# Kernel optimization log

Hardware: AMD Instinct MI355X
Metric: run time of the kernel (lower is better)

## Reference

```python
import jax, jax.numpy as jnp
import numpy as np

N = 50000          # nodes
E = 800000         # edges (before self loops)
C_IN, HID, C_OUT, L = 128, 64, 64, 3
LSTM_H = (L * HID) // 2   # 96, PyG JK-LSTM hidden size
NEG_SLOPE = 0.2


def gat_conv(x, src, dst, W, a_src, a_dst, b):
    # single-head PyG GATConv
    h = x @ W.T                                  # [N, HID]
    al = h @ a_src                               # [N] src attention logits
    ar = h @ a_dst                               # [N]
    e = jax.nn.leaky_relu(al[src] + ar[dst], NEG_SLOPE)   # [E+N]
    m = jax.ops.segment_max(e, dst, num_segments=N)
    ex = jnp.exp(e - m[dst])
    den = jax.ops.segment_sum(ex, dst, num_segments=N)
    coef = ex / den[dst]                         # segment softmax over dst neighborhoods
    out = jax.ops.segment_sum(coef[:, None] * h[src], dst, num_segments=N)
    return out + b


def lstm_dir(seq, Wih, Whh, bih, bhh, reverse):
    # seq: [L, N, C]; returns hidden states [L, N, H] in original time order
    H = Whh.shape[1]
    h0 = jnp.zeros((seq.shape[1], H), seq.dtype)

    def step(carry, x_t):
        h, c = carry
        g = x_t @ Wih.T + bih + h @ Whh.T + bhh
        i, f, gg, o = jnp.split(g, 4, axis=-1)
        c = jax.nn.sigmoid(f) * c + jax.nn.sigmoid(i) * jnp.tanh(gg)
        h = jax.nn.sigmoid(o) * jnp.tanh(c)
        return (h, c), h

    _, hs = jax.lax.scan(step, (h0, h0), seq, reverse=reverse)
    return hs


def setup_inputs() -> dict:
    key = jax.random.key(0)
    ks = jax.random.split(key, 32)
    s = 0.1
    inp = {
        'x': jax.random.normal(ks[0], (N, C_IN), jnp.float32),
        'edge_index': jax.random.randint(ks[1], (2, E), 0, N, jnp.int64
                                         if jax.config.jax_enable_x64 else jnp.int32),
    }
    dims = [C_IN, HID, HID]
    for l in range(L):
        inp[f'conv{l}_W'] = s * jax.random.normal(ks[2 + 4 * l], (HID, dims[l]), jnp.float32)
        inp[f'conv{l}_asrc'] = s * jax.random.normal(ks[3 + 4 * l], (HID,), jnp.float32)
        inp[f'conv{l}_adst'] = s * jax.random.normal(ks[4 + 4 * l], (HID,), jnp.float32)
        inp[f'conv{l}_b'] = jnp.zeros((HID,), jnp.float32)
    for d, off in (('f', 16), ('b', 20)):
        inp[f'lstm_Wih_{d}'] = s * jax.random.normal(ks[off], (4 * LSTM_H, HID), jnp.float32)
        inp[f'lstm_Whh_{d}'] = s * jax.random.normal(ks[off + 1], (4 * LSTM_H, LSTM_H), jnp.float32)
        inp[f'lstm_bih_{d}'] = jnp.zeros((4 * LSTM_H,), jnp.float32)
        inp[f'lstm_bhh_{d}'] = jnp.zeros((4 * LSTM_H,), jnp.float32)
    inp['att_W'] = s * jax.random.normal(ks[24], (1, 2 * LSTM_H), jnp.float32)
    inp['att_b'] = jnp.zeros((1,), jnp.float32)
    inp['out_W'] = s * jax.random.normal(ks[25], (C_OUT, HID), jnp.float32)
    inp['out_b'] = jnp.zeros((C_OUT,), jnp.float32)
    return inp


def reference(x, edge_index,
              conv0_W, conv0_asrc, conv0_adst, conv0_b,
              conv1_W, conv1_asrc, conv1_adst, conv1_b,
              conv2_W, conv2_asrc, conv2_adst, conv2_b,
              lstm_Wih_f, lstm_Whh_f, lstm_bih_f, lstm_bhh_f,
              lstm_Wih_b, lstm_Whh_b, lstm_bih_b, lstm_bhh_b,
              att_W, att_b, out_W, out_b):
    # add self loops (PyG GATConv default)
    loop = jnp.arange(N, dtype=edge_index.dtype)
    src = jnp.concatenate([edge_index[0], loop])
    dst = jnp.concatenate([edge_index[1], loop])

    convs = [(conv0_W, conv0_asrc, conv0_adst, conv0_b),
             (conv1_W, conv1_asrc, conv1_adst, conv1_b),
             (conv2_W, conv2_asrc, conv2_adst, conv2_b)]
    xs = []
    h = x
    for (W, asrc, adst, b) in convs:
        h = jax.nn.relu(gat_conv(h, src, dst, W, asrc, adst, b))
        xs.append(h)

    seq = jnp.stack(xs, axis=0)                       # [L, N, HID]
    hf = lstm_dir(seq, lstm_Wih_f, lstm_Whh_f, lstm_bih_f, lstm_bhh_f, False)
    hb = lstm_dir(seq, lstm_Wih_b, lstm_Whh_b, lstm_bih_b, lstm_bhh_b, True)
    hcat = jnp.concatenate([hf, hb], axis=-1)         # [L, N, 2*LSTM_H]
    logits = (hcat @ att_W.T + att_b)[..., 0]         # [L, N]
    alpha = jax.nn.softmax(logits, axis=0)            # softmax over layers
    agg = jnp.einsum('lnc,ln->nc', seq, alpha)        # [N, HID]
    return agg @ out_W.T + out_b
```

## Files before the change

kernel.cpp:

```cpp
#include <hip/hip_runtime.h>
#include <hip/hip_bf16.h>
#include <math.h>


typedef __attribute__((ext_vector_type(4))) float f32x4;
typedef __attribute__((ext_vector_type(8))) short bf16x8;

__device__ __forceinline__ float rcp_f(float x) {
    return __builtin_amdgcn_rcpf(x);
}
__device__ __forceinline__ float sigmoid_f(float x) {
    return rcp_f(1.0f + __expf(-x));
}
__device__ __forceinline__ float tanh_f(float x) {
    return fmaf(2.0f, rcp_f(1.0f + __expf(-2.0f * x)), -1.0f);
}
__device__ __forceinline__ unsigned short f2bf(float x) {
    union { float f; unsigned int u; } v; v.f = x;
    unsigned int r = (v.u + 0x7FFFu + ((v.u >> 16) & 1u)) >> 16;
    return (unsigned short)r;
}
__device__ __forceinline__ float bf2f(unsigned short u) {
    union { unsigned int i; float f; } v; v.i = ((unsigned int)u) << 16;
    return v.f;
}

template<int K>
__global__ __launch_bounds__(256) void lin_kernel(
    const float* __restrict__ x, const float* __restrict__ W,
    const float* __restrict__ asrc, const float* __restrict__ adst,
    unsigned short* __restrict__ h, float* __restrict__ al,
    float* __restrict__ ar, int N)
{
    __shared__ __align__(16) float Wl[64][K + 4];
    for (int i = threadIdx.x; i < 64 * K; i += 256)
        Wl[i / K][i % K] = W[i];
    __syncthreads();

    int lane = threadIdx.x & 63;
    float as = asrc[lane], ad = adst[lane];
    int wid = (blockIdx.x * 256 + threadIdx.x) >> 6;
    int nw  = (gridDim.x * 256) >> 6;
    int n4max = (N + 3) >> 2;
    for (int n4 = wid; n4 < n4max; n4 += nw) {
        int nb = __builtin_amdgcn_readfirstlane(n4) << 2;
        const float* xr0 = x + (size_t)nb * K;
        const float* xr1 = x + (size_t)min(nb + 1, N - 1) * K;
        const float* xr2 = x + (size_t)min(nb + 2, N - 1) * K;
        const float* xr3 = x + (size_t)min(nb + 3, N - 1) * K;
        float a0 = 0.f, a1 = 0.f, a2 = 0.f, a3 = 0.f;
        #pragma unroll 4
        for (int k = 0; k < K; k += 4) {
            f32x4 wv = *reinterpret_cast<const f32x4*>(&Wl[lane][k]);
            float4 x0 = *reinterpret_cast<const float4*>(xr0 + k);
            float4 x1 = *reinterpret_cast<const float4*>(xr1 + k);
            float4 x2 = *reinterpret_cast<const float4*>(xr2 + k);
            float4 x3 = *reinterpret_cast<const float4*>(xr3 + k);
            a0 += x0.x * wv.x + x0.y * wv.y + x0.z * wv.z + x0.w * wv.w;
            a1 += x1.x * wv.x + x1.y * wv.y + x1.z * wv.z + x1.w * wv.w;
            a2 += x2.x * wv.x + x2.y * wv.y + x2.z * wv.z + x2.w * wv.w;
            a3 += x3.x * wv.x + x3.y * wv.y + x3.z * wv.z + x3.w * wv.w;
        }
        float accs[4] = {a0, a1, a2, a3};
        #pragma unroll
        for (int j = 0; j < 4; ++j) {
            int n = nb + j;
            if (n >= N) break;
            float acc = accs[j];
            h[(size_t)n * 64 + lane] = f2bf(acc);
            float pa = acc * as, pr = acc * ad;
            #pragma unroll
            for (int off = 32; off > 0; off >>= 1) {
                pa += __shfl_down(pa, off);
                pr += __shfl_down(pr, off);
            }
            if (lane == 0) { al[n] = pa; ar[n] = pr; }
        }
    }
}

__global__ void csr_zero(int* __restrict__ deg, int* __restrict__ cursor, int N)
{
    int i = blockIdx.x * blockDim.x + threadIdx.x;
    if (i < N) { deg[i] = 0; cursor[i] = 0; }
}

__global__ void csr_hist(const int* __restrict__ dst, int* __restrict__ deg, int E)
{
    int i = blockIdx.x * blockDim.x + threadIdx.x;
    if (i < E) atomicAdd(&deg[dst[i]], 1);
}

__global__ void csr_scan1(const int* __restrict__ deg, int* __restrict__ incl,
                          int* __restrict__ part, int N)
{
    __shared__ int sb[2][256];
    int tid = threadIdx.x;
    int i = blockIdx.x * 256 + tid;
    int v = (i < N) ? deg[i] + 1 : 0;
    sb[0][tid] = v;
    __syncthreads();
    int cur = 0;
    #pragma unroll
    for (int off = 1; off < 256; off <<= 1) {
        int s = sb[cur][tid];
        if (tid >= off) s += sb[cur][tid - off];
        sb[cur ^ 1][tid] = s;
        cur ^= 1;
        __syncthreads();
    }
    if (i < N) incl[i] = sb[cur][tid];
    if (tid == 255) part[blockIdx.x] = sb[cur][255];
}

__global__ void csr_scan2(int* __restrict__ part, int NB)
{
    __shared__ int sb[2][256];
    int tid = threadIdx.x;
    int v = (tid < NB) ? part[tid] : 0;
    sb[0][tid] = v;
    __syncthreads();
    int cur = 0;
    #pragma unroll
    for (int off = 1; off < 256; off <<= 1) {
        int s = sb[cur][tid];
        if (tid >= off) s += sb[cur][tid - off];
        sb[cur ^ 1][tid] = s;
        cur ^= 1;
        __syncthreads();
    }
    if (tid < NB) part[tid] = sb[cur][tid] - v;
}

__global__ void csr_scan3(const int* __restrict__ deg, const int* __restrict__ incl,
                          const int* __restrict__ part, int* __restrict__ rowptr,
                          int N, int total)
{
    int i = blockIdx.x * blockDim.x + threadIdx.x;
    if (i < N)
        rowptr[i] = part[i >> 8] + incl[i] - (deg[i] + 1);
    if (i == 0) rowptr[N] = total;
}

__global__ void csr_scatter(const int* __restrict__ src, const int* __restrict__ dst,
                            const int* __restrict__ rowptr, int* __restrict__ cursor,
                            int* __restrict__ csr_src, int E, int N)
{
    int i = blockIdx.x * blockDim.x + threadIdx.x;
    if (i >= E + N) return;
    int s = (i < E) ? src[i] : (i - E);
    int d = (i < E) ? dst[i] : (i - E);
    int pos = atomicAdd(&cursor[d], 1);
    csr_src[rowptr[d] + pos] = s;
}

__global__ __launch_bounds__(256) void agg_kernel(
    const int* __restrict__ rowptr, const int* __restrict__ csr_src,
    const float* __restrict__ al, const float* __restrict__ ar,
    const unsigned short* __restrict__ h, const float* __restrict__ b,
    float* __restrict__ outseq, unsigned short* __restrict__ outseq_bf, int N)
{
    int lane = threadIdx.x & 63;
    int w = threadIdx.x >> 6;
    int d = blockIdx.x * 4 + w;
    if (d >= N) return;
    int li = lane & 15, grp = lane >> 4;

    int rp0 = rowptr[d], rp1 = rowptr[d + 1];
    int degd = rp1 - rp0;
    float ard = ar[d];
    float den = 0.0f;
    float a0 = 0.f, a1 = 0.f, a2 = 0.f, a3 = 0.f;

    for (int c0 = 0; c0 < degd; c0 += 64) {
        int ne = min(64, degd - c0);
        int s_l = 0;
        float ex_l = 0.0f;
        if (lane < ne) {
            s_l = csr_src[rp0 + c0 + lane];
            float e = al[s_l] + ard;
            e = (e >= 0.0f) ? e : 0.2f * e;
            ex_l = __expf(e);
        }
        float dsum = ex_l;
        #pragma unroll
        for (int off = 32; off > 0; off >>= 1) dsum += __shfl_xor(dsum, off);
        den += dsum;
        #pragma unroll 2
        for (int e2 = 0; e2 < ne; e2 += 4) {
            int eA = e2 + grp;
            float exb = __shfl(ex_l, eA);
            int sb = __shfl(s_l, eA);
            uint2 hv = *reinterpret_cast<const uint2*>(
                &h[(size_t)sb * 64 + li * 4]);
            a0 += exb * bf2f((unsigned short)(hv.x & 0xFFFFu));
            a1 += exb * bf2f((unsigned short)(hv.x >> 16));
            a2 += exb * bf2f((unsigned short)(hv.y & 0xFFFFu));
            a3 += exb * bf2f((unsigned short)(hv.y >> 16));
        }
    }
    #pragma unroll
    for (int off = 16; off < 64; off <<= 1) {
        a0 += __shfl_xor(a0, off);
        a1 += __shfl_xor(a1, off);
        a2 += __shfl_xor(a2, off);
        a3 += __shfl_xor(a3, off);
    }
    if (grp == 0) {
        float inv = rcp_f(den);
        int ch = li * 4;
        float4 v;
        v.x = fmaxf(fmaf(a0, inv, b[ch]),     0.0f);
        v.y = fmaxf(fmaf(a1, inv, b[ch + 1]), 0.0f);
        v.z = fmaxf(fmaf(a2, inv, b[ch + 2]), 0.0f);
        v.w = fmaxf(fmaf(a3, inv, b[ch + 3]), 0.0f);
        *reinterpret_cast<float4*>(&outseq[(size_t)d * 64 + ch]) = v;
        uint2 bb;
        bb.x = (unsigned int)f2bf(v.x) | ((unsigned int)f2bf(v.y) << 16);
        bb.y = (unsigned int)f2bf(v.z) | ((unsigned int)f2bf(v.w) << 16);
        *reinterpret_cast<uint2*>(&outseq_bf[(size_t)d * 64 + ch]) = bb;
    }
}

__global__ void prep_lstm(
    const float* __restrict__ WihF, const float* __restrict__ WhhF,
    const float* __restrict__ bihF, const float* __restrict__ bhhF,
    const float* __restrict__ WihB_, const float* __restrict__ WhhB_,
    const float* __restrict__ bihB_, const float* __restrict__ bhhB_,
    unsigned short* __restrict__ WB, float* __restrict__ bsum)
{
    int tid = blockIdx.x * blockDim.x + threadIdx.x;
    if (tid < 2 * 61440) {
        int dir = tid / 61440, rr = tid % 61440;
        const float* Wih = dir ? WihB_ : WihF;
        const float* Whh = dir ? WhhB_ : WhhF;
        float v;
        if (rr < 24576) {
            int f = rr >> 9, l = (rr >> 3) & 63, s = rr & 7;
            int kc = f & 1, qt = f >> 1;
            int q = qt / 6, t6 = qt % 6;
            int j = q * 96 + t6 * 16 + (l & 15);
            int k = kc * 32 + (l >> 4) * 8 + s;
            v = Wih[j * 64 + k];
        } else {
            int rr2 = rr - 24576;
            int f = rr2 >> 9, l = (rr2 >> 3) & 63, s = rr2 & 7;
            int kc = f % 3, qt = f / 3;
            int q = qt / 6, t6 = qt % 6;
            int j = q * 96 + t6 * 16 + (l & 15);
            int k = kc * 32 + (l >> 4) * 8 + s;
            v = Whh[j * 96 + k];
        }
        WB[tid] = f2bf(v);
    } else if (tid < 2 * 61440 + 2 * 384) {
        int q2 = tid - 2 * 61440;
        int dir = q2 / 384, j = q2 % 384;
        bsum[q2] = dir ? (bihB_[j] + bhhB_[j]) : (bihF[j] + bhhF[j]);
    }
}

__global__ __launch_bounds__(512, 2) void lstm_kernel(
    const unsigned short* __restrict__ seq_bf,
    const unsigned short* __restrict__ WB,
    const float* __restrict__ bsum, const float* __restrict__ attW,
    const float* __restrict__ attb, const float* __restrict__ outW,
    const float* __restrict__ outb, float* __restrict__ out, int N)
{
    __shared__ __align__(16) unsigned short smem[75520];
    unsigned short* WL = smem;
    unsigned short* HS = smem + 61440;
    float* LG = reinterpret_cast<float*>(smem + 74752);

    const int tid  = threadIdx.x;
    const int lane = tid & 63;
    const int w    = tid >> 6;
    const int i16  = lane & 15;
    const int g    = lane >> 4;
    const int n0   = blockIdx.x * 128;
    const int nodebase = 16 * w;
    const int myrow = nodebase + g * 4;

    float attb0 = attb[0];
    if (tid < 384) LG[tid] = attb0;

    for (int dir = 0; dir < 2; ++dir) {
        __syncthreads();
        {
            const f32x4* gsrc = reinterpret_cast<const f32x4*>(WB + dir * 61440);
            f32x4* ldst = reinterpret_cast<f32x4*>(WL);
            #pragma unroll
            for (int it = 0; it < 15; ++it)
                ldst[it * 512 + tid] = gsrc[it * 512 + tid];
        }
        {
            unsigned int* hz = reinterpret_cast<unsigned int*>(&HS[nodebase * 104]);
            for (int e2 = lane; e2 < 832; e2 += 64) hz[e2] = 0u;
        }
        const float* bs = bsum + dir * 384;
        const float* aw = attW + dir * 96;
        float bsr[24];
        #pragma unroll
        for (int t6 = 0; t6 < 6; ++t6)
            #pragma unroll
            for (int q = 0; q < 4; ++q)
                bsr[t6 * 4 + q] = bs[q * 96 + t6 * 16 + i16];
        float awr[6];
        #pragma unroll
        for (int t6 = 0; t6 < 6; ++t6) awr[t6] = aw[t6 * 16 + i16];
        float c[24];
        #pragma unroll
        for (int a = 0; a < 24; ++a) c[a] = 0.0f;
        __syncthreads();

        for (int step = 0; step < 3; ++step) {
            int t = dir ? (2 - step) : step;

            int nn = n0 + nodebase + i16;
            nn = (nn < N) ? nn : (N - 1);
            const unsigned short* xr = seq_bf + ((size_t)t * N + nn) * 64 + g * 8;
            bf16x8 ax0 = *reinterpret_cast<const bf16x8*>(xr);
            bf16x8 ax1 = *reinterpret_cast<const bf16x8*>(xr + 32);

            const unsigned short* hrow = &HS[(nodebase + i16) * 104];
            bf16x8 ah0 = *reinterpret_cast<const bf16x8*>(hrow + g * 8);
            bf16x8 ah1 = *reinterpret_cast<const bf16x8*>(hrow + 32 + g * 8);
            bf16x8 ah2 = *reinterpret_cast<const bf16x8*>(hrow + 64 + g * 8);
            const unsigned short* wbase = WL + lane * 8;

            float lp[4] = {0.0f, 0.0f, 0.0f, 0.0f};
            #pragma unroll
            for (int t6 = 0; t6 < 6; ++t6) {
                const int jb = t6 * 16 + i16;
                f32x4 acc4[4];
                #pragma unroll
                for (int q = 0; q < 4; ++q) {
                    float bv = bsr[t6 * 4 + q];
                    acc4[q] = (f32x4){bv, bv, bv, bv};
                }
                #pragma unroll
                for (int q = 0; q < 4; ++q) {
                    const int qt = q * 6 + t6;
                    const unsigned short* wih = wbase + (qt * 2) * 512;
                    const unsigned short* whh = wbase + 24576 + (qt * 3) * 512;
                    acc4[q] = __builtin_amdgcn_mfma_f32_16x16x32_bf16(
                        ax0, *reinterpret_cast<const bf16x8*>(wih), acc4[q], 0, 0, 0);
                    acc4[q] = __builtin_amdgcn_mfma_f32_16x16x32_bf16(
                        ax1, *reinterpret_cast<const bf16x8*>(wih + 512), acc4[q], 0, 0, 0);
                    acc4[q] = __builtin_amdgcn_mfma_f32_16x16x32_bf16(
                        ah0, *reinterpret_cast<const bf16x8*>(whh), acc4[q], 0, 0, 0);
                    acc4[q] = __builtin_amdgcn_mfma_f32_16x16x32_bf16(
                        ah1, *reinterpret_cast<const bf16x8*>(whh + 512), acc4[q], 0, 0, 0);
                    acc4[q] = __builtin_amdgcn_mfma_f32_16x16x32_bf16(
                        ah2, *reinterpret_cast<const bf16x8*>(whh + 1024), acc4[q], 0, 0, 0);
                }
                #pragma unroll
                for (int reg = 0; reg < 4; ++reg) {
                    float ii = acc4[0][reg];
                    float ff = acc4[1][reg];
                    float gg = acc4[2][reg];
                    float oo = acc4[3][reg];
                    float cn = sigmoid_f(ff) * c[t6 * 4 + reg]
                             + sigmoid_f(ii) * tanh_f(gg);
                    c[t6 * 4 + reg] = cn;
                    float hn = sigmoid_f(oo) * tanh_f(cn);
                    HS[(myrow + reg) * 104 + jb] = f2bf(hn);
                    lp[reg] += hn * awr[t6];
                }
            }
            #pragma unroll
            for (int reg = 0; reg < 4; ++reg) {
                float v = lp[reg];
                v += __shfl_xor(v, 1);
                v += __shfl_xor(v, 2);
                v += __shfl_xor(v, 4);
                v += __shfl_xor(v, 8);
                if (i16 == 0) LG[t * 128 + myrow + reg] += v;
            }
        }
    }
    __syncthreads();

    float* alphaF = reinterpret_cast<float*>(HS);
    if (tid < 128) {
        float l0 = LG[tid], l1 = LG[128 + tid], l2 = LG[256 + tid];
        float mx = fmaxf(fmaxf(l0, l1), l2);
        float e0 = __expf(l0 - mx), e1 = __expf(l1 - mx), e2 = __expf(l2 - mx);
        float inv = rcp_f(e0 + e1 + e2);
        alphaF[tid] = e0 * inv; alphaF[128 + tid] = e1 * inv;
        alphaF[256 + tid] = e2 * inv;
    }
    __syncthreads();

    float* aggF = reinterpret_cast<float*>(WL);
    for (int idx = tid; idx < 128 * 64; idx += 512) {
        int r = idx >> 6, k = idx & 63;
        int n = n0 + r;
        float v = 0.0f;
        if (n < N) {
            float a0 = alphaF[r], a1 = alphaF[128 + r], a2 = alphaF[256 + r];
            v = a0 * bf2f(seq_bf[((size_t)n) * 64 + k])
              + a1 * bf2f(seq_bf[((size_t)N + n) * 64 + k])
              + a2 * bf2f(seq_bf[((size_t)2 * N + n) * 64 + k]);
        }
        aggF[r * 68 + k] = v;
    }
    __syncthreads();

    f32x4 ow[16];
    #pragma unroll
    for (int kk = 0; kk < 16; ++kk)
        ow[kk] = *reinterpret_cast<const f32x4*>(&outW[(size_t)lane * 64 + kk * 4]);
    float ob = outb[lane];
    for (int r = w; r < 128; r += 8) {
        int n = n0 + r;
        if (n >= N) break;
        float a = ob;
        #pragma unroll
        for (int kk = 0; kk < 16; ++kk) {
            f32x4 av = *reinterpret_cast<const f32x4*>(&aggF[r * 68 + kk * 4]);
            a += ow[kk].x * av.x + ow[kk].y * av.y
               + ow[kk].z * av.z + ow[kk].w * av.w;
        }
        out[(size_t)n * 64 + lane] = a;
    }
}

extern "C" void kernel_launch(void* const* d_in, const int* in_sizes, int n_in,
                              void* d_out, int out_size, void* d_ws, size_t ws_size,
                              hipStream_t stream)
{
    const float* x    = (const float*)d_in[0];
    const int*   ei   = (const int*)d_in[1];
    const float* convW[3]  = {(const float*)d_in[2], (const float*)d_in[6],  (const float*)d_in[10]};
    const float* convAs[3] = {(const float*)d_in[3], (const float*)d_in[7],  (const float*)d_in[11]};
    const float* convAd[3] = {(const float*)d_in[4], (const float*)d_in[8],  (const float*)d_in[12]};
    const float* convB[3]  = {(const float*)d_in[5], (const float*)d_in[9],  (const float*)d_in[13]};
    const float* WihF = (const float*)d_in[14];
    const float* WhhF = (const float*)d_in[15];
    const float* bihF = (const float*)d_in[16];
    const float* bhhF = (const float*)d_in[17];
    const float* WihB = (const float*)d_in[18];
    const float* WhhB = (const float*)d_in[19];
    const float* bihB = (const float*)d_in[20];
    const float* bhhB = (const float*)d_in[21];
    const float* attW = (const float*)d_in[22];
    const float* attb = (const float*)d_in[23];
    const float* outW = (const float*)d_in[24];
    const float* outb = (const float*)d_in[25];

    int N = in_sizes[0] / 128;
    int E = in_sizes[1] / 2;
    const int* src = ei;
    const int* dst = ei + E;
    int total = E + N;

    float* w = (float*)d_ws;
    float* seq  = w;  w += (size_t)3 * N * 64;
    unsigned short* h_bf = (unsigned short*)w;  w += (size_t)N * 32;
    float* al   = w;  w += N;
    float* ar   = w;  w += N;
    float* bsum = w;  w += 768;
    unsigned short* WB = (unsigned short*)w;  w += 61440;
    unsigned short* seq_bf = (unsigned short*)w;  w += (size_t)3 * N * 32;
    int* deg     = (int*)w;        w += N;
    int* cursor  = (int*)w;        w += N;
    int* rowptr  = (int*)w;        w += (N + 1);
    int* incl    = (int*)w;        w += N;
    int* part    = (int*)w;        w += 256;
    int* csr_src = (int*)w;        w += total;

    int NB = (N + 255) / 256;

    csr_zero<<<NB, 256, 0, stream>>>(deg, cursor, N);
    csr_hist<<<(E + 255) / 256, 256, 0, stream>>>(dst, deg, E);
    csr_scan1<<<NB, 256, 0, stream>>>(deg, incl, part, N);
    csr_scan2<<<1, 256, 0, stream>>>(part, NB);
    csr_scan3<<<NB, 256, 0, stream>>>(deg, incl, part, rowptr, N, total);
    csr_scatter<<<(total + 255) / 256, 256, 0, stream>>>(src, dst, rowptr, cursor,
                                                         csr_src, E, N);

    prep_lstm<<<(2 * 61440 + 768 + 255) / 256, 256, 0, stream>>>(
        WihF, WhhF, bihF, bhhF, WihB, WhhB, bihB, bhhB, WB, bsum);

    for (int l = 0; l < 3; ++l) {
        const float* in = (l == 0) ? x : seq + (size_t)(l - 1) * N * 64;
        if (l == 0)
            lin_kernel<128><<<2048, 256, 0, stream>>>(in, convW[l], convAs[l], convAd[l],
                                                      h_bf, al, ar, N);
        else
            lin_kernel<64><<<2048, 256, 0, stream>>>(in, convW[l], convAs[l], convAd[l],
                                                     h_bf, al, ar, N);
        agg_kernel<<<(N + 3) / 4, 256, 0, stream>>>(rowptr, csr_src, al, ar, h_bf,
                                                    convB[l], seq + (size_t)l * N * 64,
                                                    seq_bf + (size_t)l * N * 64, N);
    }

    lstm_kernel<<<(N + 127) / 128, 512, 0, stream>>>(seq_bf, WB, bsum, attW, attb,
                                                     outW, outb, (float*)d_out, N);
}
```

Before: 377.2 us.

## Assign a 16-lane group per destination node in GAT aggregation

The aggregation kernel now maps four destination nodes onto each 64-lane wave, one 16-lane group per node, instead of one node per wave. Each group loads up to 16 neighbor indices at a time, reduces the softmax denominator with a 4-step group shuffle, and walks its neighbors one at a time. The final cross-group reduction of the accumulators is removed. The aim is to use more lanes when neighborhoods are small (average degree is about 17) and to cut shuffle overhead. In exchange, each group runs a longer serial gather chain, and groups in the same wave diverge when their node degrees differ.

```diff
diff --git a/kernel.cpp b/kernel.cpp
--- a/kernel.cpp
+++ b/kernel.cpp
@@ -162,35 +162,38 @@
 {
     int lane = threadIdx.x & 63;
     int w = threadIdx.x >> 6;
-    int d = blockIdx.x * 4 + w;
+    int li = lane & 15, grp = lane >> 4;
+    int d = blockIdx.x * 16 + w * 4 + grp;
     if (d >= N) return;
-    int li = lane & 15, grp = lane >> 4;
 
     int rp0 = rowptr[d], rp1 = rowptr[d + 1];
     int degd = rp1 - rp0;
     float ard = ar[d];
     float den = 0.0f;
     float a0 = 0.f, a1 = 0.f, a2 = 0.f, a3 = 0.f;
-
-    for (int c0 = 0; c0 < degd; c0 += 64) {
-        int ne = min(64, degd - c0);
+    const int grpbase = grp << 4;
+
+    for (int c0 = 0; c0 < degd; c0 += 16) {
+        int ne = min(16, degd - c0);
         int s_l = 0;
         float ex_l = 0.0f;
-        if (lane < ne) {
-            s_l = csr_src[rp0 + c0 + lane];
+        if (li < ne) {
+            s_l = csr_src[rp0 + c0 + li];
             float e = al[s_l] + ard;
             e = (e >= 0.0f) ? e : 0.2f * e;
             ex_l = __expf(e);
         }
         float dsum = ex_l;
-        #pragma unroll
-        for (int off = 32; off > 0; off >>= 1) dsum += __shfl_xor(dsum, off);
+        dsum += __shfl_xor(dsum, 1);
+        dsum += __shfl_xor(dsum, 2);
+        dsum += __shfl_xor(dsum, 4);
+        dsum += __shfl_xor(dsum, 8);
         den += dsum;
-        #pragma unroll 2
-        for (int e2 = 0; e2 < ne; e2 += 4) {
-            int eA = e2 + grp;
-            float exb = __shfl(ex_l, eA);
-            int sb = __shfl(s_l, eA);
+        #pragma unroll 4
+        for (int e2 = 0; e2 < ne; ++e2) {
+            int sl = grpbase + e2;
+            float exb = __shfl(ex_l, sl);
+            int sb = __shfl(s_l, sl);
             uint2 hv = *reinterpret_cast<const uint2*>(
                 &h[(size_t)sb * 64 + li * 4]);
             a0 += exb * bf2f((unsigned short)(hv.x & 0xFFFFu));
@@ -199,27 +202,18 @@
             a3 += exb * bf2f((unsigned short)(hv.y >> 16));
         }
     }
-    #pragma unroll
-    for (int off = 16; off < 64; off <<= 1) {
-        a0 += __shfl_xor(a0, off);
-        a1 += __shfl_xor(a1, off);
-        a2 += __shfl_xor(a2, off);
-        a3 += __shfl_xor(a3, off);
-    }
-    if (grp == 0) {
-        float inv = rcp_f(den);
-        int ch = li * 4;
-        float4 v;
-        v.x = fmaxf(fmaf(a0, inv, b[ch]),     0.0f);
-        v.y = fmaxf(fmaf(a1, inv, b[ch + 1]), 0.0f);
-        v.z = fmaxf(fmaf(a2, inv, b[ch + 2]), 0.0f);
-        v.w = fmaxf(fmaf(a3, inv, b[ch + 3]), 0.0f);
-        *reinterpret_cast<float4*>(&outseq[(size_t)d * 64 + ch]) = v;
-        uint2 bb;
-        bb.x = (unsigned int)f2bf(v.x) | ((unsigned int)f2bf(v.y) << 16);
-        bb.y = (unsigned int)f2bf(v.z) | ((unsigned int)f2bf(v.w) << 16);
-        *reinterpret_cast<uint2*>(&outseq_bf[(size_t)d * 64 + ch]) = bb;
-    }
+    float inv = rcp_f(den);
+    int ch = li * 4;
+    float4 v;
+    v.x = fmaxf(fmaf(a0, inv, b[ch]),     0.0f);
+    v.y = fmaxf(fmaf(a1, inv, b[ch + 1]), 0.0f);
+    v.z = fmaxf(fmaf(a2, inv, b[ch + 2]), 0.0f);
+    v.w = fmaxf(fmaf(a3, inv, b[ch + 3]), 0.0f);
+    *reinterpret_cast<float4*>(&outseq[(size_t)d * 64 + ch]) = v;
+    uint2 bb;
+    bb.x = (unsigned int)f2bf(v.x) | ((unsigned int)f2bf(v.y) << 16);
+    bb.y = (unsigned int)f2bf(v.z) | ((unsigned int)f2bf(v.w) << 16);
+    *reinterpret_cast<uint2*>(&outseq_bf[(size_t)d * 64 + ch]) = bb;
 }
 
 __global__ void prep_lstm(
@@ -490,9 +484,9 @@
         else
             lin_kernel<64><<<2048, 256, 0, stream>>>(in, convW[l], convAs[l], convAd[l],
                                                      h_bf, al, ar, N);
-        agg_kernel<<<(N + 3) / 4, 256, 0, stream>>>(rowptr, csr_src, al, ar, h_bf,
-                                                    convB[l], seq + (size_t)l * N * 64,
-                                                    seq_bf + (size_t)l * N * 64, N);
+        agg_kernel<<<(N + 15) / 16, 256, 0, stream>>>(rowptr, csr_src, al, ar, h_bf,
+                                                      convB[l], seq + (size_t)l * N * 64,
+                                                      seq_bf + (size_t)l * N * 64, N);
     }
 
     lstm_kernel<<<(N + 127) / 128, 512, 0, stream>>>(seq_bf, WB, bsum, attW, attb,
```

Result: no change. 374.1 us, median of 2 (-0.8%).
